# Performance work log

Measured on AMD Instinct MI355X. Metric: run time of the kernel, lower is better.

## Reference

```python
import jax, jax.numpy as jnp
import numpy as np

B, N, IN_DIM, OUT_DIM, K = 64, 256, 512, 512, 8
DK = OUT_DIM // K  # per-kernel feature dim


def setup_inputs() -> dict:
    key = jax.random.key(0)
    k1, k2, k3, k4 = jax.random.split(key, 4)
    node_feats = jax.random.normal(k1, (B, N, IN_DIM), dtype=jnp.float32)
    adj = jax.random.uniform(k2, (B, K, N, N), dtype=jnp.float32)
    weight = jax.random.normal(k3, (IN_DIM, OUT_DIM), dtype=jnp.float32) * (1.0 / np.sqrt(IN_DIM))
    bias = jax.random.normal(k4, (OUT_DIM,), dtype=jnp.float32) * 0.01
    return {"node_feats": node_feats, "adj": adj, "weight": weight, "bias": bias}


def reference(node_feats, adj, weight, bias):
    # kernel linear + ReLU: (b, n, out_dim)
    h = jax.nn.relu(jnp.einsum('bni,io->bno', node_feats, weight) + bias)
    # split into kernel slots: (b, n, k, dk)
    h = h.reshape(B, N, K, DK)
    # graph.aggregate: per-kernel dense message passing over adjacency
    # out[b,n,k,d] = sum_m adj[b,k,n,m] * h[b,m,k,d]
    agg = jnp.einsum('bknm,bmkd->bnkd', adj, h)
    return agg.reshape(B, N, OUT_DIM)
```

## Files before the change

### kernel.cpp

```cpp
#include <hip/hip_runtime.h>
#include <hip/hip_bf16.h>


typedef __attribute__((ext_vector_type(8))) short short8;
typedef __attribute__((ext_vector_type(4))) float floatx4;

__device__ __forceinline__ unsigned short f2bf(float f) {
    union { float f; unsigned u; } v; v.f = f;
    unsigned r = v.u + 0x7FFFu + ((v.u >> 16) & 1u);
    return (unsigned short)(r >> 16);
}

__device__ __forceinline__ unsigned pk2bf(float a, float b) {
    union { __hip_bfloat162 h; unsigned u; } cv;
    cv.h = __float22bfloat162_rn(make_float2(a, b));
    return cv.u;
}

__global__ __launch_bounds__(256) void wt_kernel(const float* __restrict__ W,
                                                 unsigned short* __restrict__ Wt) {
    __shared__ unsigned short t_lds[64 * 66];
    const int tile = blockIdx.x;
    const int k0 = (tile >> 3) * 64;
    const int o0 = (tile & 7) * 64;
    const int t = threadIdx.x;
    const int c = t & 63;
    const int rb = t >> 6;
#pragma unroll
    for (int i = 0; i < 16; ++i) {
        int r = i * 4 + rb;
        t_lds[c * 66 + r] = f2bf(W[(size_t)(k0 + r) * 512 + o0 + c]);
    }
    __syncthreads();
#pragma unroll
    for (int i = 0; i < 16; ++i) {
        int o_r = i * 4 + rb;
        Wt[(size_t)(o0 + o_r) * 512 + k0 + c] = t_lds[o_r * 66 + c];
    }
}

__global__ __launch_bounds__(1024, 8) void fused_kernel(
    const float* __restrict__ X, const unsigned short* __restrict__ Wt,
    const float* __restrict__ bias, const float* __restrict__ adj,
    float* __restrict__ out) {
    __shared__ union {
        struct {
            unsigned short a[256 * 40];
            unsigned short w[64 * 40];
        } s1;
        unsigned short ht[64 * 264];
    } lds;

    const int id = blockIdx.x;
    const int b = id & 63;
    const int ks = id >> 6;

    const int tid = threadIdx.x;
    const int lane = tid & 63, w = tid >> 6;
    const int lrow = lane & 15, quad = lane >> 4;

    const float* Xb = X + (size_t)b * 256 * 512;
    const unsigned short* Wslice = Wt + (size_t)ks * 64 * 512;

    floatx4 acc1[4];
    const floatx4 fzero = {0.f, 0.f, 0.f, 0.f};
#pragma unroll
    for (int j = 0; j < 4; ++j) acc1[j] = fzero;

    for (int kb = 0; kb < 16; ++kb) {
        const int k0 = kb * 32;
#pragma unroll
        for (int i = 0; i < 2; ++i) {
            int c4 = tid + i * 1024;
            int rr = c4 >> 3;
            int cc = (c4 & 7) * 4;
            const float4 v = *(const float4*)(Xb + (size_t)rr * 512 + k0 + cc);
            unsigned p01 = pk2bf(v.x, v.y);
            unsigned p23 = pk2bf(v.z, v.w);
            unsigned* dst = (unsigned*)(lds.s1.a + rr * 40 + cc);
            dst[0] = p01; dst[1] = p23;
        }
        if (tid < 512) {
            int rr = tid >> 3;
            int cc = (tid & 7) * 4;
            *(ushort4*)(lds.s1.w + rr * 40 + cc) =
                *(const ushort4*)(Wslice + (size_t)rr * 512 + k0 + cc);
        }
        __syncthreads();

        short8 af, bfr[4];
        af = *(const short8*)(lds.s1.a + (w * 16 + lrow) * 40 + quad * 8);
#pragma unroll
        for (int j = 0; j < 4; ++j)
            bfr[j] = *(const short8*)(lds.s1.w + (16 * j + lrow) * 40 + quad * 8);
#pragma unroll
        for (int j = 0; j < 4; ++j)
            acc1[j] = __builtin_amdgcn_mfma_f32_16x16x32_bf16(af, bfr[j], acc1[j], 0, 0, 0);
        __syncthreads();
    }

#pragma unroll
    for (int j = 0; j < 4; ++j) {
        int d = 16 * j + lrow;
        float bv = bias[ks * 64 + d];
        int m = w * 16 + quad * 4;
        floatx4 c = acc1[j];
        unsigned p01 = pk2bf(fmaxf(c.x + bv, 0.f), fmaxf(c.y + bv, 0.f));
        unsigned p23 = pk2bf(fmaxf(c.z + bv, 0.f), fmaxf(c.w + bv, 0.f));
        unsigned* d32 = (unsigned*)(lds.ht + d * 264 + m);
        d32[0] = p01; d32[1] = p23;
    }
    __syncthreads();

    const float* Abase = adj + ((size_t)(b * 8 + ks)) * 65536;
    const float* A0 = Abase + (size_t)(w * 16 + lrow) * 256;

    floatx4 acc2[4];
#pragma unroll
    for (int j = 0; j < 4; ++j) acc2[j] = fzero;

#pragma unroll
    for (int mt = 0; mt < 8; ++mt) {
        const int m0 = mt * 32 + quad * 8;
        const float* src = A0 + m0;
        float4 v0 = *(const float4*)src;
        float4 v1 = *(const float4*)(src + 4);
        union { short8 s; unsigned u[4]; } t;
        t.u[0] = pk2bf(v0.x, v0.y);
        t.u[1] = pk2bf(v0.z, v0.w);
        t.u[2] = pk2bf(v1.x, v1.y);
        t.u[3] = pk2bf(v1.z, v1.w);
        short8 af = t.s;
        short8 bfr[4];
#pragma unroll
        for (int j = 0; j < 4; ++j)
            bfr[j] = *(const short8*)(lds.ht + (16 * j + lrow) * 264 + m0);
#pragma unroll
        for (int j = 0; j < 4; ++j)
            acc2[j] = __builtin_amdgcn_mfma_f32_16x16x32_bf16(af, bfr[j], acc2[j], 0, 0, 0);
    }

#pragma unroll
    for (int j = 0; j < 4; ++j) {
        int n = w * 16 + quad * 4;
        int d = 16 * j + lrow;
        float* dst = out + ((size_t)b * 256 + n) * 512 + ks * 64 + d;
        floatx4 c = acc2[j];
        dst[0 * 512] = c.x;
        dst[1 * 512] = c.y;
        dst[2 * 512] = c.z;
        dst[3 * 512] = c.w;
    }
}

extern "C" void kernel_launch(void* const* d_in, const int* in_sizes, int n_in,
                              void* d_out, int out_size, void* d_ws, size_t ws_size,
                              hipStream_t stream) {
    const float* X    = (const float*)d_in[0];
    const float* adj  = (const float*)d_in[1];
    const float* W    = (const float*)d_in[2];
    const float* bias = (const float*)d_in[3];
    float* out = (float*)d_out;

    unsigned short* Wt = (unsigned short*)d_ws;

    wt_kernel<<<64, 256, 0, stream>>>(W, Wt);
    fused_kernel<<<512, 1024, 0, stream>>>(X, Wt, bias, adj, out);
}
```

Before: 253.4 us.

## Stage adjacency tiles through swizzled LDS for coalesced loads in aggregation

The aggregation phase now loads the adjacency matrix in four 64-row tiles. All threads cooperatively read each tile with contiguous loads, convert it to bf16 and write it into an XOR-swizzled LDS buffer. The MFMA operands are then read back from LDS. The ReLU'd hidden tile is also moved from a padded layout to a swizzled one to avoid bank conflicts. The aim is better global coalescing and fewer LDS conflicts. In exchange it adds barriers and serializes the four tile phases, which lowers memory-level parallelism compared with the fully unrolled direct loads.

```diff
diff --git a/kernel.cpp b/kernel.cpp
--- a/kernel.cpp
+++ b/kernel.cpp
@@ -48,7 +48,10 @@
             unsigned short a[256 * 40];
             unsigned short w[64 * 40];
         } s1;
-        unsigned short ht[64 * 264];
+        struct {
+            unsigned short ht[64 * 256];
+            unsigned short at[64 * 256];
+        } s2;
     } lds;
 
     const int id = blockIdx.x;
@@ -107,49 +110,52 @@
         floatx4 c = acc1[j];
         unsigned p01 = pk2bf(fmaxf(c.x + bv, 0.f), fmaxf(c.y + bv, 0.f));
         unsigned p23 = pk2bf(fmaxf(c.z + bv, 0.f), fmaxf(c.w + bv, 0.f));
-        unsigned* d32 = (unsigned*)(lds.ht + d * 264 + m);
+        int jm = 2 * w + (quad >> 1);
+        int phys = jm ^ (d & 7);
+        unsigned* d32 = (unsigned*)(lds.s2.ht + d * 256 + phys * 8 + (quad & 1) * 4);
         d32[0] = p01; d32[1] = p23;
     }
     __syncthreads();
 
     const float* Abase = adj + ((size_t)(b * 8 + ks)) * 65536;
-    const float* A0 = Abase + (size_t)(w * 16 + lrow) * 256;
+    const int wn = w & 3, wd = w >> 2;
 
-    floatx4 acc2[4];
+    for (int nt = 0; nt < 4; ++nt) {
 #pragma unroll
-    for (int j = 0; j < 4; ++j) acc2[j] = fzero;
+        for (int s = 0; s < 2; ++s) {
+            int c = s * 1024 + tid;
+            int nl = c >> 5;
+            int jm = c & 31;
+            const float* src = Abase + ((size_t)(nt * 64 + nl)) * 256 + jm * 8;
+            float4 v0 = *(const float4*)src;
+            float4 v1 = *(const float4*)(src + 4);
+            union { short8 sh; unsigned u[4]; } t;
+            t.u[0] = pk2bf(v0.x, v0.y);
+            t.u[1] = pk2bf(v0.z, v0.w);
+            t.u[2] = pk2bf(v1.x, v1.y);
+            t.u[3] = pk2bf(v1.z, v1.w);
+            *(short8*)(lds.s2.at + nl * 256 + ((jm ^ (nl & 7)) * 8)) = t.sh;
+        }
+        __syncthreads();
 
+        floatx4 acc = fzero;
+        const int nl = wn * 16 + lrow;
+        const int d  = wd * 16 + lrow;
 #pragma unroll
-    for (int mt = 0; mt < 8; ++mt) {
-        const int m0 = mt * 32 + quad * 8;
-        const float* src = A0 + m0;
-        float4 v0 = *(const float4*)src;
-        float4 v1 = *(const float4*)(src + 4);
-        union { short8 s; unsigned u[4]; } t;
-        t.u[0] = pk2bf(v0.x, v0.y);
-        t.u[1] = pk2bf(v0.z, v0.w);
-        t.u[2] = pk2bf(v1.x, v1.y);
-        t.u[3] = pk2bf(v1.z, v1.w);
-        short8 af = t.s;
-        short8 bfr[4];
-#pragma unroll
-        for (int j = 0; j < 4; ++j)
-            bfr[j] = *(const short8*)(lds.ht + (16 * j + lrow) * 264 + m0);
-#pragma unroll
-        for (int j = 0; j < 4; ++j)
-            acc2[j] = __builtin_amdgcn_mfma_f32_16x16x32_bf16(af, bfr[j], acc2[j], 0, 0, 0);
-    }
+        for (int mt = 0; mt < 8; ++mt) {
+            int jm = 4 * mt + quad;
+            short8 afr = *(const short8*)(lds.s2.at + nl * 256 + ((jm ^ (lrow & 7)) * 8));
+            short8 bfr = *(const short8*)(lds.s2.ht + d  * 256 + ((jm ^ (lrow & 7)) * 8));
+            acc = __builtin_amdgcn_mfma_f32_16x16x32_bf16(afr, bfr, acc, 0, 0, 0);
+        }
+        __syncthreads();
 
-#pragma unroll
-    for (int j = 0; j < 4; ++j) {
-        int n = w * 16 + quad * 4;
-        int d = 16 * j + lrow;
-        float* dst = out + ((size_t)b * 256 + n) * 512 + ks * 64 + d;
-        floatx4 c = acc2[j];
-        dst[0 * 512] = c.x;
-        dst[1 * 512] = c.y;
-        dst[2 * 512] = c.z;
-        dst[3 * 512] = c.w;
+        int n_g = nt * 64 + wn * 16 + quad * 4;
+        float* dst = out + ((size_t)b * 256 + n_g) * 512 + ks * 64 + wd * 16 + lrow;
+        dst[0 * 512] = acc.x;
+        dst[1 * 512] = acc.y;
+        dst[2 * 512] = acc.z;
+        dst[3 * 512] = acc.w;
     }
 }
 
```

Measured after the change: 249.4 us. About the same (-1.6%).
